# Kernel tuning notes

Hardware: AMD Instinct MI355X
Metric: run time of the kernel (lower is better)

## Reference

```python
import jax, jax.numpy as jnp
import numpy as np

MARGIN = 1.0


def setup_inputs() -> dict:
    key = jax.random.key(0)
    k1, k2, k3 = jax.random.split(key, 3)
    n, d = 8192, 128
    feat1 = jax.random.normal(k1, (n, d), dtype=jnp.float32)
    feat2 = jax.random.normal(k2, (n, d), dtype=jnp.float32)
    # similarity labels in {+1, -1}, as expected by HingeEmbeddingLoss
    simi = (2 * jax.random.randint(k3, (n, n), 0, 2) - 1).astype(jnp.int32)
    return {"feat1": feat1, "feat2": feat2, "simi": simi}


def reference(feat1, feat2, simi):
    # logits[i,j] = -||feat1_i - feat2_j||^2, computed without the O(n*m*d) expand
    sq1 = jnp.sum(feat1 * feat1, axis=-1, keepdims=True)          # [n, 1]
    sq2 = jnp.sum(feat2 * feat2, axis=-1)                          # [m]
    cross = jnp.einsum('nd,md->nm', feat1, feat2)                  # [n, m]
    logits = -(sq1 + sq2[None, :] - 2.0 * cross)                   # [n, m]
    probs = jax.nn.softmax(logits, axis=1)                         # [n, m]
    # HingeEmbeddingLoss: x if y==1 else max(0, margin - x); mean reduction
    loss = jnp.where(simi == 1, probs, jnp.maximum(0.0, MARGIN - probs))
    return jnp.mean(loss)
```

## Files before the change

### kernel.cpp

```cpp
#include <hip/hip_runtime.h>
#include <hip/hip_bf16.h>
#include <stdint.h>

#define N 8192
#define D 128
#define NCHUNK 16
#define CHUNK (N / NCHUNK)
#define RT 128
#define CT 64
#define NTILES (CHUNK / CT)

typedef short bf16x8 __attribute__((ext_vector_type(8)));
typedef float f32x4 __attribute__((ext_vector_type(4)));
typedef unsigned int uint32;
typedef unsigned long long uint64;

#define OFF_ACC   0u
#define OFF_SQ2   1024u
#define OFF_RPOS  (OFF_SQ2 + N * 4u)
#define OFF_M     (OFF_RPOS + N * 4u)
#define OFF_L     (OFF_M + NCHUNK * N * 4u)
#define OFF_S     (OFF_L + NCHUNK * N * 4u)
#define OFF_F1    (OFF_S + NCHUNK * N * 4u)
#define OFF_F2    (OFF_F1 + N * D * 2u)
#define OFF_PACK  (OFF_F2 + N * D * 2u)

__global__ __launch_bounds__(256)
void prep_kernel(const float* __restrict__ f1, const float* __restrict__ f2,
                 unsigned short* __restrict__ f1b, unsigned short* __restrict__ f2b,
                 float* __restrict__ sq2) {
    const int w    = blockIdx.x * 4 + (threadIdx.x >> 6);
    const int lane = threadIdx.x & 63;
    for (int row = w; row < N; row += 1024) {
        float a0 = f1[row * D + lane];
        float a1 = f1[row * D + 64 + lane];
        float b0 = f2[row * D + lane];
        float b1 = f2[row * D + 64 + lane];
        __hip_bfloat16 t;
        t = __float2bfloat16(a0); f1b[row * D + lane]      = *(unsigned short*)&t;
        t = __float2bfloat16(a1); f1b[row * D + 64 + lane] = *(unsigned short*)&t;
        t = __float2bfloat16(b0); f2b[row * D + lane]      = *(unsigned short*)&t;
        t = __float2bfloat16(b1); f2b[row * D + 64 + lane] = *(unsigned short*)&t;
        float ss = b0 * b0 + b1 * b1;
        #pragma unroll
        for (int off = 32; off > 0; off >>= 1) ss += __shfl_xor(ss, off);
        if (lane == 0) sq2[row] = ss;
    }
}

__global__ __launch_bounds__(256)
void pack_kernel(const int* __restrict__ simi, uint64* __restrict__ packed,
                 uint32* __restrict__ rowpos) {
    const int wave = threadIdx.x >> 6;
    const int lane = threadIdx.x & 63;
    const int row  = blockIdx.x * 4 + wave;
    const int* rp = simi + (size_t)row * N;
    uint64* dstrow = packed + (size_t)row * (N / 64);
    uint32 pos = 0;
    int v[16];
    #pragma unroll
    for (int i = 0; i < 16; i++) v[i] = rp[i * 64 + lane];
    #pragma unroll
    for (int g = 0; g < 8; g++) {
        int w[16];
        if (g < 7) {
            #pragma unroll
            for (int i = 0; i < 16; i++) w[i] = rp[(g + 1) * 1024 + i * 64 + lane];
        }
        uint64 b[16];
        #pragma unroll
        for (int i = 0; i < 16; i++) b[i] = __ballot(v[i] == 1);
        if (lane == 0) {
            #pragma unroll
            for (int i = 0; i < 8; i++) {
                ulonglong2 p = {b[2 * i], b[2 * i + 1]};
                *reinterpret_cast<ulonglong2*>(dstrow + g * 16 + 2 * i) = p;
            }
            #pragma unroll
            for (int i = 0; i < 16; i++) pos += (uint32)__popcll(b[i]);
        }
        if (g < 7) {
            #pragma unroll
            for (int i = 0; i < 16; i++) v[i] = w[i];
        }
    }
    if (lane == 0) rowpos[row] = pos;
}

__global__ __launch_bounds__(256)
void main_kernel(const unsigned short* __restrict__ f1b,
                 const unsigned short* __restrict__ f2b,
                 const float* __restrict__ sq2,
                 const uint32* __restrict__ packed32,
                 float* __restrict__ pm, float* __restrict__ pl, float* __restrict__ ps) {
    __shared__ unsigned short ldsB[CT * D];
    __shared__ float ldsSq[CHUNK];

    const int tid  = threadIdx.x;
    const int wave = tid >> 6;
    const int lane = tid & 63;
    const int lo   = lane & 15;
    const int hi   = lane >> 4;

    const int rowtile = blockIdx.x;
    const int chunk   = blockIdx.y;
    const int rbase   = rowtile * RT + wave * 32;
    const int cbase0  = chunk * CHUNK;

    for (int i = tid; i < CHUNK; i += 256) ldsSq[i] = sq2[cbase0 + i];

    bf16x8 afrag[2][4];
    #pragma unroll
    for (int a = 0; a < 2; a++) {
        const unsigned short* ap = f1b + (size_t)(rbase + a * 16 + lo) * D + hi * 8;
        #pragma unroll
        for (int kk = 0; kk < 4; kk++)
            afrag[a][kk] = *reinterpret_cast<const bf16x8*>(ap + kk * 32);
    }

    const int sq_ = (tid >> 4);
    const int sg_ = tid & 15;

    const uint32* pk = packed32 + (size_t)(rbase + hi * 4) * (N / 32)
                                + (cbase0 >> 5) + (lo >> 3);
    const int mshift = 4 * (lo & 7);

    float m[2][4], l[2][4], s[2][4];
    #pragma unroll
    for (int a = 0; a < 2; a++)
        #pragma unroll
        for (int r = 0; r < 4; r++) { m[a][r] = -1e30f; l[a][r] = 0.f; s[a][r] = 0.f; }

    for (int t = 0; t < NTILES; t++) {
        const int cbase = cbase0 + t * CT;

        uint32 mb[2][4];
        #pragma unroll
        for (int a = 0; a < 2; a++)
            #pragma unroll
            for (int r = 0; r < 4; r++)
                mb[a][r] = (pk[(size_t)(a * 16 + r) * (N / 32)] >> mshift) & 0xfu;

        __syncthreads();
        #pragma unroll
        for (int it = 0; it < 4; it++) {
            int q = it * 16 + sq_;
            int c = 4 * (q & 15) + (q >> 4);
            const uint4 v = *reinterpret_cast<const uint4*>(f2b + (size_t)(cbase + c) * D + sg_ * 8);
            *reinterpret_cast<uint4*>(ldsB + q * D + ((sg_ ^ (q & 15)) * 8)) = v;
        }
        __syncthreads();

        f32x4 acc[2][4];
        #pragma unroll
        for (int cf = 0; cf < 4; cf++) {
            acc[0][cf] = (f32x4){0.f, 0.f, 0.f, 0.f};
            acc[1][cf] = (f32x4){0.f, 0.f, 0.f, 0.f};
            const int brow = cf * 16 + lo;
            #pragma unroll
            for (int kk = 0; kk < 4; kk++) {
                int g = kk * 4 + hi;
                bf16x8 b = *reinterpret_cast<const bf16x8*>(
                    ldsB + brow * D + ((g ^ (brow & 15)) * 8));
                acc[0][cf] = __builtin_amdgcn_mfma_f32_16x16x32_bf16(afrag[0][kk], b, acc[0][cf], 0, 0, 0);
                acc[1][cf] = __builtin_amdgcn_mfma_f32_16x16x32_bf16(afrag[1][kk], b, acc[1][cf], 0, 0, 0);
            }
        }

        f32x4 sqv = *reinterpret_cast<const f32x4*>(&ldsSq[t * CT + 4 * lo]);
        #pragma unroll
        for (int a = 0; a < 2; a++)
            #pragma unroll
            for (int r = 0; r < 4; r++) {
                float lg[4];
                #pragma unroll
                for (int cf = 0; cf < 4; cf++)
                    lg[cf] = 2.0f * acc[a][cf][r] - sqv[cf];
                float tm = fmaxf(fmaxf(lg[0], lg[1]), fmaxf(lg[2], lg[3]));
                float mn = fmaxf(m[a][r], tm);
                float al = __expf(m[a][r] - mn);
                m[a][r] = mn;
                float p[4];
                #pragma unroll
                for (int cf = 0; cf < 4; cf++) p[cf] = __expf(lg[cf] - mn);
                l[a][r] = l[a][r] * al + ((p[0] + p[1]) + (p[2] + p[3]));
                float sm = 0.f;
                #pragma unroll
                for (int cf = 0; cf < 4; cf++)
                    sm += ((mb[a][r] >> cf) & 1u) ? p[cf] : 0.f;
                s[a][r] = s[a][r] * al + sm;
            }
        pk += 2;
    }

    #pragma unroll
    for (int a = 0; a < 2; a++)
        #pragma unroll
        for (int r = 0; r < 4; r++) {
            float M = m[a][r];
            #pragma unroll
            for (int off = 1; off < 16; off <<= 1)
                M = fmaxf(M, __shfl_xor(M, off));
            float sc = __expf(m[a][r] - M);
            float L = l[a][r] * sc, S = s[a][r] * sc;
            #pragma unroll
            for (int off = 1; off < 16; off <<= 1) {
                L += __shfl_xor(L, off);
                S += __shfl_xor(S, off);
            }
            if (lo == 0) {
                int row = rbase + a * 16 + hi * 4 + r;
                int idx = chunk * N + row;
                pm[idx] = M; pl[idx] = L; ps[idx] = S;
            }
        }
}

__global__ void merge_kernel(const float* __restrict__ pm, const float* __restrict__ pl,
                             const float* __restrict__ ps, const uint32* __restrict__ rowpos,
                             float* __restrict__ s_acc, uint32* __restrict__ pos_acc) {
    const int row = blockIdx.x * 256 + threadIdx.x;
    float M = -1e30f;
    #pragma unroll
    for (int k = 0; k < NCHUNK; k++) M = fmaxf(M, pm[k * N + row]);
    float L = 0.f, S = 0.f;
    #pragma unroll
    for (int k = 0; k < NCHUNK; k++) {
        float e = __expf(pm[k * N + row] - M);
        L += pl[k * N + row] * e;
        S += ps[k * N + row] * e;
    }
    float r = S / L;
    uint32 pc = rowpos[row];
    #pragma unroll
    for (int off = 32; off > 0; off >>= 1) {
        r  += __shfl_xor(r, off);
        pc += __shfl_xor(pc, off);
    }
    __shared__ float red[4];
    __shared__ uint32 redp[4];
    int lane = threadIdx.x & 63, w = threadIdx.x >> 6;
    if (lane == 0) { red[w] = r; redp[w] = pc; }
    __syncthreads();
    if (threadIdx.x == 0) {
        atomicAdd(s_acc, red[0] + red[1] + red[2] + red[3]);
        atomicAdd(pos_acc, redp[0] + redp[1] + redp[2] + redp[3]);
    }
}

__global__ void final_kernel(const float* __restrict__ s_acc, const uint32* __restrict__ pos_acc,
                             float* __restrict__ out) {
    double S = (double)s_acc[0];
    double C = (double)N * (double)N - (double)pos_acc[0];
    double n = (double)N;
    out[0] = (float)((2.0 * S + C - n) / (n * n));
}

extern "C" void kernel_launch(void* const* d_in, const int* in_sizes, int n_in,
                              void* d_out, int out_size, void* d_ws, size_t ws_size,
                              hipStream_t stream) {
    const float* f1   = (const float*)d_in[0];
    const float* f2   = (const float*)d_in[1];
    const int*   simi = (const int*)d_in[2];
    float* out = (float*)d_out;
    char* ws = (char*)d_ws;

    float*  acc_s  = (float*)(ws + OFF_ACC);
    uint32* acc_p  = (uint32*)(ws + OFF_ACC + 4);
    float*  sq2    = (float*)(ws + OFF_SQ2);
    uint32* rowpos = (uint32*)(ws + OFF_RPOS);
    float*  pm     = (float*)(ws + OFF_M);
    float*  pl     = (float*)(ws + OFF_L);
    float*  ps     = (float*)(ws + OFF_S);
    unsigned short* f1b = (unsigned short*)(ws + OFF_F1);
    unsigned short* f2b = (unsigned short*)(ws + OFF_F2);
    uint64* packed = (uint64*)(ws + OFF_PACK);

    hipMemsetAsync(ws + OFF_ACC, 0, 64, stream);
    prep_kernel<<<256, 256, 0, stream>>>(f1, f2, f1b, f2b, sq2);
    pack_kernel<<<N / 4, 256, 0, stream>>>(simi, packed, rowpos);
    main_kernel<<<dim3(N / RT, NCHUNK), 256, 0, stream>>>(f1b, f2b, sq2,
                                                          (const uint32*)packed, pm, pl, ps);
    merge_kernel<<<N / 256, 256, 0, stream>>>(pm, pl, ps, rowpos, acc_s, acc_p);
    final_kernel<<<1, 1, 0, stream>>>(acc_s, acc_p, out);
}
```

Measured before the change: 420.8 us.

## Fuse label packing into main kernel, reading int32 labels directly

Removes the separate pack kernel that turned the int32 similarity matrix into a bitmask. The main kernel now loads int4 label vectors straight from the input, builds the per-column nibble masks in registers, and counts negative labels per block for the merge step. It also drops the LDS staging of squared norms in favour of direct global loads. This saves one kernel launch and the write and reread of the packed mask, but the main kernel now streams the full 256 MB label matrix with strided int4 loads interleaved with the MFMA work, so it may become memory-bound.

```diff
diff --git a/kernel.cpp b/kernel.cpp
--- a/kernel.cpp
+++ b/kernel.cpp
@@ -9,21 +9,20 @@
 #define RT 128
 #define CT 64
 #define NTILES (CHUNK / CT)
+#define NBLK (N / RT * NCHUNK)
 
 typedef short bf16x8 __attribute__((ext_vector_type(8)));
 typedef float f32x4 __attribute__((ext_vector_type(4)));
 typedef unsigned int uint32;
-typedef unsigned long long uint64;
 
 #define OFF_ACC   0u
 #define OFF_SQ2   1024u
-#define OFF_RPOS  (OFF_SQ2 + N * 4u)
-#define OFF_M     (OFF_RPOS + N * 4u)
+#define OFF_BCNT  (OFF_SQ2 + N * 4u)
+#define OFF_M     (OFF_BCNT + NBLK * 4u)
 #define OFF_L     (OFF_M + NCHUNK * N * 4u)
 #define OFF_S     (OFF_L + NCHUNK * N * 4u)
 #define OFF_F1    (OFF_S + NCHUNK * N * 4u)
 #define OFF_F2    (OFF_F1 + N * D * 2u)
-#define OFF_PACK  (OFF_F2 + N * D * 2u)
 
 __global__ __launch_bounds__(256)
 void prep_kernel(const float* __restrict__ f1, const float* __restrict__ f2,
@@ -49,52 +48,14 @@
 }
 
 __global__ __launch_bounds__(256)
-void pack_kernel(const int* __restrict__ simi, uint64* __restrict__ packed,
-                 uint32* __restrict__ rowpos) {
-    const int wave = threadIdx.x >> 6;
-    const int lane = threadIdx.x & 63;
-    const int row  = blockIdx.x * 4 + wave;
-    const int* rp = simi + (size_t)row * N;
-    uint64* dstrow = packed + (size_t)row * (N / 64);
-    uint32 pos = 0;
-    int v[16];
-    #pragma unroll
-    for (int i = 0; i < 16; i++) v[i] = rp[i * 64 + lane];
-    #pragma unroll
-    for (int g = 0; g < 8; g++) {
-        int w[16];
-        if (g < 7) {
-            #pragma unroll
-            for (int i = 0; i < 16; i++) w[i] = rp[(g + 1) * 1024 + i * 64 + lane];
-        }
-        uint64 b[16];
-        #pragma unroll
-        for (int i = 0; i < 16; i++) b[i] = __ballot(v[i] == 1);
-        if (lane == 0) {
-            #pragma unroll
-            for (int i = 0; i < 8; i++) {
-                ulonglong2 p = {b[2 * i], b[2 * i + 1]};
-                *reinterpret_cast<ulonglong2*>(dstrow + g * 16 + 2 * i) = p;
-            }
-            #pragma unroll
-            for (int i = 0; i < 16; i++) pos += (uint32)__popcll(b[i]);
-        }
-        if (g < 7) {
-            #pragma unroll
-            for (int i = 0; i < 16; i++) v[i] = w[i];
-        }
-    }
-    if (lane == 0) rowpos[row] = pos;
-}
-
-__global__ __launch_bounds__(256)
 void main_kernel(const unsigned short* __restrict__ f1b,
                  const unsigned short* __restrict__ f2b,
                  const float* __restrict__ sq2,
-                 const uint32* __restrict__ packed32,
-                 float* __restrict__ pm, float* __restrict__ pl, float* __restrict__ ps) {
+                 const int* __restrict__ simi,
+                 float* __restrict__ pm, float* __restrict__ pl, float* __restrict__ ps,
+                 uint32* __restrict__ blockcnt) {
     __shared__ unsigned short ldsB[CT * D];
-    __shared__ float ldsSq[CHUNK];
+    __shared__ uint32 cred[4];
 
     const int tid  = threadIdx.x;
     const int wave = tid >> 6;
@@ -107,8 +68,6 @@
     const int rbase   = rowtile * RT + wave * 32;
     const int cbase0  = chunk * CHUNK;
 
-    for (int i = tid; i < CHUNK; i += 256) ldsSq[i] = sq2[cbase0 + i];
-
     bf16x8 afrag[2][4];
     #pragma unroll
     for (int a = 0; a < 2; a++) {
@@ -121,25 +80,24 @@
     const int sq_ = (tid >> 4);
     const int sg_ = tid & 15;
 
-    const uint32* pk = packed32 + (size_t)(rbase + hi * 4) * (N / 32)
-                                + (cbase0 >> 5) + (lo >> 3);
-    const int mshift = 4 * (lo & 7);
+    const int* simi_p = simi + (size_t)(rbase + hi * 4) * N + cbase0 + 4 * lo;
 
     float m[2][4], l[2][4], s[2][4];
     #pragma unroll
     for (int a = 0; a < 2; a++)
         #pragma unroll
         for (int r = 0; r < 4; r++) { m[a][r] = -1e30f; l[a][r] = 0.f; s[a][r] = 0.f; }
+    uint32 cnt = 0;
 
     for (int t = 0; t < NTILES; t++) {
         const int cbase = cbase0 + t * CT;
 
-        uint32 mb[2][4];
+        int4 mkv[2][4];
         #pragma unroll
         for (int a = 0; a < 2; a++)
             #pragma unroll
             for (int r = 0; r < 4; r++)
-                mb[a][r] = (pk[(size_t)(a * 16 + r) * (N / 32)] >> mshift) & 0xfu;
+                mkv[a][r] = *reinterpret_cast<const int4*>(simi_p + (size_t)(a * 16 + r) * N);
 
         __syncthreads();
         #pragma unroll
@@ -151,6 +109,18 @@
         }
         __syncthreads();
 
+        uint32 mb[2][4];
+        #pragma unroll
+        for (int a = 0; a < 2; a++)
+            #pragma unroll
+            for (int r = 0; r < 4; r++) {
+                int4 v = mkv[a][r];
+                uint32 nib = (uint32)(v.x == 1) | ((uint32)(v.y == 1) << 1) |
+                             ((uint32)(v.z == 1) << 2) | ((uint32)(v.w == 1) << 3);
+                mb[a][r] = nib;
+                cnt += 4u - __popc(nib);
+            }
+
         f32x4 acc[2][4];
         #pragma unroll
         for (int cf = 0; cf < 4; cf++) {
@@ -167,7 +137,7 @@
             }
         }
 
-        f32x4 sqv = *reinterpret_cast<const f32x4*>(&ldsSq[t * CT + 4 * lo]);
+        f32x4 sqv = *reinterpret_cast<const f32x4*>(sq2 + cbase0 + t * CT + 4 * lo);
         #pragma unroll
         for (int a = 0; a < 2; a++)
             #pragma unroll
@@ -190,7 +160,7 @@
                     sm += ((mb[a][r] >> cf) & 1u) ? p[cf] : 0.f;
                 s[a][r] = s[a][r] * al + sm;
             }
-        pk += 2;
+        simi_p += CT;
     }
 
     #pragma unroll
@@ -214,11 +184,18 @@
                 pm[idx] = M; pl[idx] = L; ps[idx] = S;
             }
         }
+
+    #pragma unroll
+    for (int off = 1; off < 64; off <<= 1) cnt += __shfl_xor(cnt, off);
+    if (lane == 0) cred[wave] = cnt;
+    __syncthreads();
+    if (tid == 0)
+        blockcnt[blockIdx.y * 64 + blockIdx.x] = cred[0] + cred[1] + cred[2] + cred[3];
 }
 
 __global__ void merge_kernel(const float* __restrict__ pm, const float* __restrict__ pl,
-                             const float* __restrict__ ps, const uint32* __restrict__ rowpos,
-                             float* __restrict__ s_acc, uint32* __restrict__ pos_acc) {
+                             const float* __restrict__ ps, const uint32* __restrict__ blockcnt,
+                             float* __restrict__ s_acc, uint32* __restrict__ neg_acc) {
     const int row = blockIdx.x * 256 + threadIdx.x;
     float M = -1e30f;
     #pragma unroll
@@ -231,7 +208,7 @@
         S += ps[k * N + row] * e;
     }
     float r = S / L;
-    uint32 pc = rowpos[row];
+    uint32 pc = (threadIdx.x < 32) ? blockcnt[blockIdx.x * 32 + threadIdx.x] : 0u;
     #pragma unroll
     for (int off = 32; off > 0; off >>= 1) {
         r  += __shfl_xor(r, off);
@@ -244,14 +221,14 @@
     __syncthreads();
     if (threadIdx.x == 0) {
         atomicAdd(s_acc, red[0] + red[1] + red[2] + red[3]);
-        atomicAdd(pos_acc, redp[0] + redp[1] + redp[2] + redp[3]);
-    }
-}
-
-__global__ void final_kernel(const float* __restrict__ s_acc, const uint32* __restrict__ pos_acc,
+        atomicAdd(neg_acc, redp[0] + redp[1] + redp[2] + redp[3]);
+    }
+}
+
+__global__ void final_kernel(const float* __restrict__ s_acc, const uint32* __restrict__ neg_acc,
                              float* __restrict__ out) {
     double S = (double)s_acc[0];
-    double C = (double)N * (double)N - (double)pos_acc[0];
+    double C = (double)neg_acc[0];
     double n = (double)N;
     out[0] = (float)((2.0 * S + C - n) / (n * n));
 }
@@ -265,22 +242,20 @@
     float* out = (float*)d_out;
     char* ws = (char*)d_ws;
 
-    float*  acc_s  = (float*)(ws + OFF_ACC);
-    uint32* acc_p  = (uint32*)(ws + OFF_ACC + 4);
-    float*  sq2    = (float*)(ws + OFF_SQ2);
-    uint32* rowpos = (uint32*)(ws + OFF_RPOS);
-    float*  pm     = (float*)(ws + OFF_M);
-    float*  pl     = (float*)(ws + OFF_L);
-    float*  ps     = (float*)(ws + OFF_S);
+    float*  acc_s    = (float*)(ws + OFF_ACC);
+    uint32* acc_n    = (uint32*)(ws + OFF_ACC + 4);
+    float*  sq2      = (float*)(ws + OFF_SQ2);
+    uint32* blockcnt = (uint32*)(ws + OFF_BCNT);
+    float*  pm       = (float*)(ws + OFF_M);
+    float*  pl       = (float*)(ws + OFF_L);
+    float*  ps       = (float*)(ws + OFF_S);
     unsigned short* f1b = (unsigned short*)(ws + OFF_F1);
     unsigned short* f2b = (unsigned short*)(ws + OFF_F2);
-    uint64* packed = (uint64*)(ws + OFF_PACK);
 
     hipMemsetAsync(ws + OFF_ACC, 0, 64, stream);
     prep_kernel<<<256, 256, 0, stream>>>(f1, f2, f1b, f2b, sq2);
-    pack_kernel<<<N / 4, 256, 0, stream>>>(simi, packed, rowpos);
-    main_kernel<<<dim3(N / RT, NCHUNK), 256, 0, stream>>>(f1b, f2b, sq2,
-                                                          (const uint32*)packed, pm, pl, ps);
-    merge_kernel<<<N / 256, 256, 0, stream>>>(pm, pl, ps, rowpos, acc_s, acc_p);
-    final_kernel<<<1, 1, 0, stream>>>(acc_s, acc_p, out);
-}
+    main_kernel<<<dim3(N / RT, NCHUNK), 256, 0, stream>>>(f1b, f2b, sq2, simi,
+                                                          pm, pl, ps, blockcnt);
+    merge_kernel<<<N / 256, 256, 0, stream>>>(pm, pl, ps, blockcnt, acc_s, acc_n);
+    final_kernel<<<1, 1, 0, stream>>>(acc_s, acc_n, out);
+}
```

Result: faster. 405.9 us (-3.5%).
